# Kernel tuning notes

Hardware: AMD Instinct MI355X
Metric: run time of the kernel (lower is better)

The kernel has to match this reference:

```python
import jax, jax.numpy as jnp
import numpy as np

DIM = 512
QK_DIM = 128
HIDDEN = 2 * DIM  # expansion_factor * dim
EPS = 1e-5


def layernorm(x, scale, bias):
    mu = jnp.mean(x, axis=-1, keepdims=True)
    var = jnp.mean((x - mu) ** 2, axis=-1, keepdims=True)
    return (x - mu) * jax.lax.rsqrt(var + EPS) * scale + bias


def setup_inputs() -> dict:
    key = jax.random.key(0)
    ks = jax.random.split(key, 8)
    b, s = 4, 4096
    x = jax.random.normal(ks[0], (b, s, DIM), dtype=jnp.float32)
    inv = lambda fan_in: 1.0 / np.sqrt(fan_in)
    W_hidden = jax.random.normal(ks[1], (DIM, 2 * HIDDEN), dtype=jnp.float32) * inv(DIM)
    b_hidden = jnp.zeros((2 * HIDDEN,), dtype=jnp.float32)
    W_qk = jax.random.normal(ks[2], (DIM, QK_DIM), dtype=jnp.float32) * inv(DIM)
    b_qk = jnp.zeros((QK_DIM,), dtype=jnp.float32)
    gamma = jax.random.normal(ks[3], (2, QK_DIM), dtype=jnp.float32) * 0.02
    beta = jnp.zeros((2, QK_DIM), dtype=jnp.float32)
    W_out = jax.random.normal(ks[4], (HIDDEN, DIM), dtype=jnp.float32) * inv(HIDDEN)
    b_out = jnp.zeros((DIM,), dtype=jnp.float32)
    norm_scale = jnp.ones((DIM,), dtype=jnp.float32)
    norm_bias = jnp.zeros((DIM,), dtype=jnp.float32)
    return {
        "x": x,
        "norm_scale": norm_scale,
        "norm_bias": norm_bias,
        "W_hidden": W_hidden,
        "b_hidden": b_hidden,
        "W_qk": W_qk,
        "b_qk": b_qk,
        "gamma": gamma,
        "beta": beta,
        "W_out": W_out,
        "b_out": b_out,
    }


def reference(x, norm_scale, norm_bias, W_hidden, b_hidden, W_qk, b_qk, gamma, beta, W_out, b_out):
    seq_len = x.shape[-2]
    normed = layernorm(x, norm_scale, norm_bias)
    hidden = jax.nn.silu(normed @ W_hidden + b_hidden)          # [b, s, 2*hidden]
    v, gate = jnp.split(hidden, 2, axis=-1)                      # each [b, s, hidden]
    Z = jax.nn.silu(normed @ W_qk + b_qk)                        # [b, s, qk]
    QK = Z[..., None, :] * gamma + beta                          # [b, s, 2, qk]
    q = QK[..., 0, :]
    k = QK[..., 1, :]
    sim = jnp.einsum('bid,bjd->bij', q, k) / seq_len             # [b, s, s]
    A = jnp.square(jax.nn.relu(sim))
    V = jnp.einsum('bij,bjd->bid', A, v) * gate                  # [b, s, hidden]
    out = V @ W_out + b_out
    return out + x
```

## Files before the change

### kernel.cpp

```cpp
#include <hip/hip_runtime.h>
#include <cstdint>
#include <cstddef>

#define DIM   512
#define QKD   128
#define HID   1024
#define SEQ   4096
#define BAT   4
#define TOK   (BAT*SEQ)

typedef float f32x4 __attribute__((ext_vector_type(4)));
typedef int   i32x4 __attribute__((ext_vector_type(4)));
typedef int   i32x8 __attribute__((ext_vector_type(8)));

__device__ __forceinline__ unsigned short f2b(float f) {
    unsigned u = __builtin_bit_cast(unsigned, f);
    u += 0x7FFFu + ((u >> 16) & 1u);
    return (unsigned short)(u >> 16);
}
__device__ __forceinline__ float b2f(unsigned short h) {
    return __builtin_bit_cast(float, ((unsigned)h) << 16);
}
__device__ __forceinline__ float silu_f(float x) { return x / (1.f + __expf(-x)); }

__device__ __forceinline__ unsigned char f2e4(float f) {
    int v = __builtin_amdgcn_cvt_pk_fp8_f32(f, 0.f, 0, false);
    return (unsigned char)(v & 0xff);
}
__device__ __forceinline__ unsigned f2e4x4(float a, float b, float c, float d) {
    int w = __builtin_amdgcn_cvt_pk_fp8_f32(a, b, 0, false);
    w = __builtin_amdgcn_cvt_pk_fp8_f32(c, d, w, true);
    return (unsigned)w;
}

__device__ __forceinline__ void load16_lds(const void* gp, void* lp) {
    __builtin_amdgcn_global_load_lds(
        (const __attribute__((address_space(1))) unsigned int*)gp,
        (__attribute__((address_space(3))) unsigned int*)lp,
        16, 0, 0);
}

__global__ __launch_bounds__(256) void ln_kernel(
    const float* __restrict__ x, const float* __restrict__ sc,
    const float* __restrict__ bi, unsigned char* __restrict__ out)
{
    const int lane = threadIdx.x & 63, wid = threadIdx.x >> 6;
    const int row  = blockIdx.x * 4 + wid;
    const float4* xr = (const float4*)(x + (size_t)row * DIM);
    float4 a = xr[lane], b = xr[64 + lane];
    float s = a.x + a.y + a.z + a.w + b.x + b.y + b.z + b.w;
    float q = a.x*a.x + a.y*a.y + a.z*a.z + a.w*a.w
            + b.x*b.x + b.y*b.y + b.z*b.z + b.w*b.w;
#pragma unroll
    for (int m = 1; m < 64; m <<= 1) { s += __shfl_xor(s, m); q += __shfl_xor(q, m); }
    const float mean = s * (1.f / DIM);
    const float var  = q * (1.f / DIM) - mean * mean;
    const float rs   = rsqrtf(var + 1e-5f);
    float4 s0 = ((const float4*)sc)[lane], s1 = ((const float4*)sc)[64 + lane];
    float4 b0 = ((const float4*)bi)[lane], b1 = ((const float4*)bi)[64 + lane];
    unsigned wlo = f2e4x4((a.x - mean) * rs * s0.x + b0.x,
                          (a.y - mean) * rs * s0.y + b0.y,
                          (a.z - mean) * rs * s0.z + b0.z,
                          (a.w - mean) * rs * s0.w + b0.w);
    unsigned whi = f2e4x4((b.x - mean) * rs * s1.x + b1.x,
                          (b.y - mean) * rs * s1.y + b1.y,
                          (b.z - mean) * rs * s1.z + b1.z,
                          (b.w - mean) * rs * s1.w + b1.w);
    unsigned char* orow = out + (size_t)row * DIM;
    *(unsigned*)(orow + 4 * lane)       = wlo;
    *(unsigned*)(orow + 256 + 4 * lane) = whi;
}

__global__ __launch_bounds__(256) void tcast_f2e4_kernel(
    const float* __restrict__ in, unsigned char* __restrict__ out, int R, int C)
{
    __shared__ float t[32][33];
    const int tx = threadIdx.x & 31, ty = threadIdx.x >> 5;
    const int c0 = blockIdx.x * 32, r0 = blockIdx.y * 32;
#pragma unroll
    for (int i = 0; i < 4; ++i)
        t[ty + i * 8][tx] = in[(size_t)(r0 + ty + i * 8) * C + c0 + tx];
    __syncthreads();
#pragma unroll
    for (int i = 0; i < 4; ++i)
        out[(size_t)(c0 + ty + i * 8) * R + r0 + tx] = f2e4(t[tx][ty + i * 8] * 16.f);
}

__global__ __launch_bounds__(256) void copy_kernel(
    const float* __restrict__ in, float* __restrict__ out, int n4)
{
    int i = blockIdx.x * 256 + threadIdx.x;
    int stride = gridDim.x * 256;
    for (; i < n4; i += stride)
        ((float4*)out)[i] = ((const float4*)in)[i];
}

template<int EPI>
__global__ __launch_bounds__(256) void gemm8(
    const unsigned char* __restrict__ A, const unsigned char* __restrict__ B,
    int K, long strAz, long strBz, long strOz,
    const float* __restrict__ f0, const float* __restrict__ f1,
    const float* __restrict__ f2, const float* __restrict__ f3,
    const float* __restrict__ f4, const float* __restrict__ f5,
    unsigned short* __restrict__ gate,
    unsigned char* __restrict__ o0, unsigned char* __restrict__ o1,
    unsigned char* __restrict__ o2,
    float* __restrict__ fo, float scale)
{
    __shared__ unsigned char lds[32768];
    const int tid  = threadIdx.x;
    const int m0   = blockIdx.y * 128, n0 = blockIdx.x * 128;
    const int z    = blockIdx.z;
    A += (size_t)z * strAz;  B += (size_t)z * strBz;
    const int lane = tid & 63, wid = tid >> 6;
    const int wm   = (wid & 1) * 64, wn = (wid >> 1) * 64;
    const int l15  = lane & 15, quad = lane >> 4;

    f32x4 acc[4][4] = {};

    const int srow = tid >> 3, sseg = tid & 7;
    const unsigned char* gA = A + (size_t)(m0 + srow) * K + sseg * 16;
    const unsigned char* gB = B + (size_t)(n0 + srow) * K + sseg * 16;
    unsigned char* lA = lds + (size_t)tid * 16;
    unsigned char* lB = lds + 16384 + (size_t)tid * 16;

    for (int kt = 0; kt < K; kt += 128) {
#pragma unroll
        for (int i = 0; i < 4; ++i)
            load16_lds(gA + (size_t)i * 32 * K + kt, lA + i * 4096);
#pragma unroll
        for (int i = 0; i < 4; ++i)
            load16_lds(gB + (size_t)i * 32 * K + kt, lB + i * 4096);
        __syncthreads();
        i32x4 alo[4], ahi[4], blo[4], bhi[4];
#pragma unroll
        for (int mi = 0; mi < 4; ++mi) {
            const unsigned char* p = lds + (wm + mi * 16 + l15) * 128 + quad * 32;
            alo[mi] = *(const i32x4*)p; ahi[mi] = *(const i32x4*)(p + 16);
        }
#pragma unroll
        for (int ni = 0; ni < 4; ++ni) {
            const unsigned char* p = lds + 16384 + (wn + ni * 16 + l15) * 128 + quad * 32;
            blo[ni] = *(const i32x4*)p; bhi[ni] = *(const i32x4*)(p + 16);
        }
#pragma unroll
        for (int mi = 0; mi < 4; ++mi) {
            i32x8 af = __builtin_shufflevector(alo[mi], ahi[mi], 0,1,2,3,4,5,6,7);
#pragma unroll
            for (int ni = 0; ni < 4; ++ni) {
                i32x8 bf = __builtin_shufflevector(blo[ni], bhi[ni], 0,1,2,3,4,5,6,7);
                acc[mi][ni] = __builtin_amdgcn_mfma_scale_f32_16x16x128_f8f6f4(
                    af, bf, acc[mi][ni], 0, 0,
                    0, 0x7F7F7F7F, 0, 0x7F7F7F7F);
            }
        }
        __syncthreads();
    }

#pragma unroll
    for (int mi = 0; mi < 4; ++mi)
#pragma unroll
    for (int ni = 0; ni < 4; ++ni) {
        const int grow0 = m0 + wm + mi * 16 + quad * 4;
        const int gcol  = n0 + wn + ni * 16 + l15;
        if constexpr (EPI == 0) {
            if (gcol < HID) {
                const int b = grow0 >> 12, rloc = grow0 & (SEQ - 1);
                unsigned w = f2e4x4(silu_f(acc[mi][ni][0] * 0.0625f + f0[gcol]),
                                    silu_f(acc[mi][ni][1] * 0.0625f + f0[gcol]),
                                    silu_f(acc[mi][ni][2] * 0.0625f + f0[gcol]),
                                    silu_f(acc[mi][ni][3] * 0.0625f + f0[gcol]));
                *(unsigned*)(o0 + (size_t)b * HID * SEQ + (size_t)gcol * SEQ + rloc) = w;
            } else if (gcol < 2048) {
#pragma unroll
                for (int r = 0; r < 4; ++r)
                    gate[(size_t)(grow0 + r) * HID + (gcol - HID)] =
                        f2b(silu_f(acc[mi][ni][r] * 0.0625f + f0[gcol]));
            } else {
                const int c = gcol - 2048;
#pragma unroll
                for (int r = 0; r < 4; ++r) {
                    float zf = silu_f(acc[mi][ni][r] * 0.0625f + f1[c]);
                    o1[(size_t)(grow0 + r) * QKD + c] = f2e4((zf * f2[c] + f4[c]) * 64.f);
                    o2[(size_t)(grow0 + r) * QKD + c] = f2e4((zf * f3[c] + f5[c]) * 64.f);
                }
            }
        } else if constexpr (EPI == 1) {
            unsigned char* Ao = o0 + (size_t)z * strOz;
#pragma unroll
            for (int r = 0; r < 4; ++r) {
                float t = fmaxf(acc[mi][ni][r], 0.f) * 0.0625f;
                Ao[(size_t)(grow0 + r) * SEQ + gcol] = f2e4(t * t);
            }
        } else if constexpr (EPI == 2) {
            unsigned short* gz = gate + (size_t)z * strOz;
            unsigned char*  vo = o0 + (size_t)z * strOz;
#pragma unroll
            for (int r = 0; r < 4; ++r) {
                float g = b2f(gz[(size_t)(grow0 + r) * HID + gcol]);
                vo[(size_t)(grow0 + r) * HID + gcol] = f2e4(acc[mi][ni][r] * scale * g);
            }
        } else {
#pragma unroll
            for (int r = 0; r < 4; ++r)
                fo[(size_t)(grow0 + r) * DIM + gcol] =
                    acc[mi][ni][r] * scale + f0[gcol] + f1[(size_t)(grow0 + r) * DIM + gcol];
        }
    }
}

extern "C" void kernel_launch(void* const* d_in, const int* in_sizes, int n_in,
                              void* d_out, int out_size, void* d_ws, size_t ws_size,
                              hipStream_t stream) {
    const float* x     = (const float*)d_in[0];
    const float* nsc   = (const float*)d_in[1];
    const float* nbi   = (const float*)d_in[2];
    const float* Wh    = (const float*)d_in[3];
    const float* bh    = (const float*)d_in[4];
    const float* Wqk   = (const float*)d_in[5];
    const float* bqk   = (const float*)d_in[6];
    const float* gamma = (const float*)d_in[7];
    const float* beta  = (const float*)d_in[8];
    const float* Wout  = (const float*)d_in[9];
    const float* bout  = (const float*)d_in[10];
    float* out = (float*)d_out;

    uint8_t* ws = (uint8_t*)d_ws;
    size_t off = 0;
    auto alloc = [&](size_t n) { uint8_t* p = ws + off; off += (n + 255) & ~(size_t)255; return p; };
    unsigned char*  normed8 = (unsigned char*) alloc((size_t)TOK * DIM);
    unsigned char*  Wc8     = (unsigned char*) alloc((size_t)2176 * DIM);
    unsigned char*  Wout8   = (unsigned char*) alloc((size_t)DIM * HID);
    unsigned char*  vT8     = (unsigned char*) alloc((size_t)BAT * HID * SEQ);
    unsigned short* gbuf    = (unsigned short*)alloc((size_t)TOK * HID * 2);
    unsigned char*  q8      = (unsigned char*) alloc((size_t)TOK * QKD);
    unsigned char*  k8      = (unsigned char*) alloc((size_t)TOK * QKD);
    unsigned char*  Ab8     = (unsigned char*) alloc((size_t)BAT * SEQ * SEQ);
    unsigned char*  vg8     = (unsigned char*) alloc((size_t)TOK * HID);

    if (ws_size < off) {
        copy_kernel<<<4096, 256, 0, stream>>>(x, out, TOK * DIM / 4);
        return;
    }

    ln_kernel<<<TOK / 4, 256, 0, stream>>>(x, nsc, nbi, normed8);
    tcast_f2e4_kernel<<<dim3(2048 / 32, DIM / 32), 256, 0, stream>>>(Wh, Wc8, DIM, 2048);
    tcast_f2e4_kernel<<<dim3(QKD / 32, DIM / 32), 256, 0, stream>>>(
        Wqk, Wc8 + (size_t)2048 * DIM, DIM, QKD);
    tcast_f2e4_kernel<<<dim3(DIM / 32, HID / 32), 256, 0, stream>>>(Wout, Wout8, HID, DIM);

    gemm8<0><<<dim3(2176 / 128, TOK / 128), 256, 0, stream>>>(
        normed8, Wc8, DIM, 0, 0, 0,
        bh, bqk, gamma, gamma + QKD, beta, beta + QKD,
        gbuf, vT8, q8, k8, nullptr, 0.f);

    gemm8<1><<<dim3(SEQ / 128, SEQ / 128, BAT), 256, 0, stream>>>(
        q8, k8, QKD, (long)SEQ * QKD, (long)SEQ * QKD, (long)SEQ * SEQ,
        nullptr, nullptr, nullptr, nullptr, nullptr, nullptr,
        nullptr, Ab8, nullptr, nullptr, nullptr, 0.f);

    gemm8<2><<<dim3(HID / 128, SEQ / 128, BAT), 256, 0, stream>>>(
        Ab8, vT8, SEQ, (long)SEQ * SEQ, (long)HID * SEQ, (long)SEQ * HID,
        nullptr, nullptr, nullptr, nullptr, nullptr, nullptr,
        gbuf, vg8, nullptr, nullptr, nullptr, 0x1p-12f);

    gemm8<3><<<dim3(DIM / 128, TOK / 128), 256, 0, stream>>>(
        vg8, Wout8, HID, 0, 0, 0,
        bout, x, nullptr, nullptr, nullptr, nullptr,
        nullptr, nullptr, nullptr, nullptr, out, 0x1p-32f);
}
```

Before: 314.3 us.

## Template GEMM on K-tile depth, swizzle block order, store gate as fp8

```diff
diff --git a/kernel.cpp b/kernel.cpp
--- a/kernel.cpp
+++ b/kernel.cpp
@@ -18,9 +18,6 @@
     u += 0x7FFFu + ((u >> 16) & 1u);
     return (unsigned short)(u >> 16);
 }
-__device__ __forceinline__ float b2f(unsigned short h) {
-    return __builtin_bit_cast(float, ((unsigned)h) << 16);
-}
 __device__ __forceinline__ float silu_f(float x) { return x / (1.f + __expf(-x)); }
 
 __device__ __forceinline__ unsigned char f2e4(float f) {
@@ -31,6 +28,9 @@
     int w = __builtin_amdgcn_cvt_pk_fp8_f32(a, b, 0, false);
     w = __builtin_amdgcn_cvt_pk_fp8_f32(c, d, w, true);
     return (unsigned)w;
+}
+__device__ __forceinline__ float e42f(unsigned char b) {
+    return __builtin_amdgcn_cvt_f32_fp8((int)b, 0);
 }
 
 __device__ __forceinline__ void load16_lds(const void* gp, void* lp) {
@@ -95,22 +95,29 @@
         ((float4*)out)[i] = ((const float4*)in)[i];
 }
 
-template<int EPI>
+template<int EPI, int BK, int NX>
 __global__ __launch_bounds__(256) void gemm8(
     const unsigned char* __restrict__ A, const unsigned char* __restrict__ B,
     int K, long strAz, long strBz, long strOz,
     const float* __restrict__ f0, const float* __restrict__ f1,
     const float* __restrict__ f2, const float* __restrict__ f3,
     const float* __restrict__ f4, const float* __restrict__ f5,
-    unsigned short* __restrict__ gate,
+    unsigned char* __restrict__ gate,
     unsigned char* __restrict__ o0, unsigned char* __restrict__ o1,
     unsigned char* __restrict__ o2,
     float* __restrict__ fo, float scale)
 {
-    __shared__ unsigned char lds[32768];
-    const int tid  = threadIdx.x;
-    const int m0   = blockIdx.y * 128, n0 = blockIdx.x * 128;
-    const int z    = blockIdx.z;
+    constexpr int TPR = BK / 16;
+    constexpr int RPI = 256 / TPR;
+    constexpr int NIS = 128 / RPI;
+    __shared__ unsigned char lds[2 * 128 * BK];
+
+    const int tid = threadIdx.x;
+    const int d  = blockIdx.x + NX * blockIdx.y;
+    const int qd = d >> 3;
+    const int m0 = ((d & 7) + 8 * (qd / NX)) * 128;
+    const int n0 = (qd % NX) * 128;
+    const int z  = blockIdx.z;
     A += (size_t)z * strAz;  B += (size_t)z * strBz;
     const int lane = tid & 63, wid = tid >> 6;
     const int wm   = (wid & 1) * 64, wn = (wid >> 1) * 64;
@@ -118,40 +125,43 @@
 
     f32x4 acc[4][4] = {};
 
-    const int srow = tid >> 3, sseg = tid & 7;
+    const int srow = tid / TPR, sseg = tid % TPR;
     const unsigned char* gA = A + (size_t)(m0 + srow) * K + sseg * 16;
     const unsigned char* gB = B + (size_t)(n0 + srow) * K + sseg * 16;
     unsigned char* lA = lds + (size_t)tid * 16;
-    unsigned char* lB = lds + 16384 + (size_t)tid * 16;
-
-    for (int kt = 0; kt < K; kt += 128) {
-#pragma unroll
-        for (int i = 0; i < 4; ++i)
-            load16_lds(gA + (size_t)i * 32 * K + kt, lA + i * 4096);
-#pragma unroll
-        for (int i = 0; i < 4; ++i)
-            load16_lds(gB + (size_t)i * 32 * K + kt, lB + i * 4096);
+    unsigned char* lB = lds + 128 * BK + (size_t)tid * 16;
+
+    for (int kt = 0; kt < K; kt += BK) {
+#pragma unroll
+        for (int i = 0; i < NIS; ++i)
+            load16_lds(gA + (size_t)i * RPI * K + kt, lA + i * 4096);
+#pragma unroll
+        for (int i = 0; i < NIS; ++i)
+            load16_lds(gB + (size_t)i * RPI * K + kt, lB + i * 4096);
         __syncthreads();
-        i32x4 alo[4], ahi[4], blo[4], bhi[4];
-#pragma unroll
-        for (int mi = 0; mi < 4; ++mi) {
-            const unsigned char* p = lds + (wm + mi * 16 + l15) * 128 + quad * 32;
-            alo[mi] = *(const i32x4*)p; ahi[mi] = *(const i32x4*)(p + 16);
-        }
-#pragma unroll
-        for (int ni = 0; ni < 4; ++ni) {
-            const unsigned char* p = lds + 16384 + (wn + ni * 16 + l15) * 128 + quad * 32;
-            blo[ni] = *(const i32x4*)p; bhi[ni] = *(const i32x4*)(p + 16);
-        }
-#pragma unroll
-        for (int mi = 0; mi < 4; ++mi) {
-            i32x8 af = __builtin_shufflevector(alo[mi], ahi[mi], 0,1,2,3,4,5,6,7);
+#pragma unroll
+        for (int kk = 0; kk < BK; kk += 128) {
+            i32x4 alo[4], ahi[4], blo[4], bhi[4];
+#pragma unroll
+            for (int mi = 0; mi < 4; ++mi) {
+                const unsigned char* p = lds + (size_t)(wm + mi * 16 + l15) * BK + kk + quad * 32;
+                alo[mi] = *(const i32x4*)p; ahi[mi] = *(const i32x4*)(p + 16);
+            }
 #pragma unroll
             for (int ni = 0; ni < 4; ++ni) {
-                i32x8 bf = __builtin_shufflevector(blo[ni], bhi[ni], 0,1,2,3,4,5,6,7);
-                acc[mi][ni] = __builtin_amdgcn_mfma_scale_f32_16x16x128_f8f6f4(
-                    af, bf, acc[mi][ni], 0, 0,
-                    0, 0x7F7F7F7F, 0, 0x7F7F7F7F);
+                const unsigned char* p = lds + 128 * BK + (size_t)(wn + ni * 16 + l15) * BK + kk + quad * 32;
+                blo[ni] = *(const i32x4*)p; bhi[ni] = *(const i32x4*)(p + 16);
+            }
+#pragma unroll
+            for (int mi = 0; mi < 4; ++mi) {
+                i32x8 af = __builtin_shufflevector(alo[mi], ahi[mi], 0,1,2,3,4,5,6,7);
+#pragma unroll
+                for (int ni = 0; ni < 4; ++ni) {
+                    i32x8 bf = __builtin_shufflevector(blo[ni], bhi[ni], 0,1,2,3,4,5,6,7);
+                    acc[mi][ni] = __builtin_amdgcn_mfma_scale_f32_16x16x128_f8f6f4(
+                        af, bf, acc[mi][ni], 0, 0,
+                        0, 0x7F7F7F7F, 0, 0x7F7F7F7F);
+                }
             }
         }
         __syncthreads();
@@ -175,7 +185,7 @@
 #pragma unroll
                 for (int r = 0; r < 4; ++r)
                     gate[(size_t)(grow0 + r) * HID + (gcol - HID)] =
-                        f2b(silu_f(acc[mi][ni][r] * 0.0625f + f0[gcol]));
+                        f2e4(silu_f(acc[mi][ni][r] * 0.0625f + f0[gcol]));
             } else {
                 const int c = gcol - 2048;
 #pragma unroll
@@ -193,11 +203,11 @@
                 Ao[(size_t)(grow0 + r) * SEQ + gcol] = f2e4(t * t);
             }
         } else if constexpr (EPI == 2) {
-            unsigned short* gz = gate + (size_t)z * strOz;
-            unsigned char*  vo = o0 + (size_t)z * strOz;
+            unsigned char* gz = gate + (size_t)z * strOz;
+            unsigned char* vo = o0 + (size_t)z * strOz;
 #pragma unroll
             for (int r = 0; r < 4; ++r) {
-                float g = b2f(gz[(size_t)(grow0 + r) * HID + gcol]);
+                float g = e42f(gz[(size_t)(grow0 + r) * HID + gcol]);
                 vo[(size_t)(grow0 + r) * HID + gcol] = f2e4(acc[mi][ni][r] * scale * g);
             }
         } else {
@@ -228,15 +238,15 @@
     uint8_t* ws = (uint8_t*)d_ws;
     size_t off = 0;
     auto alloc = [&](size_t n) { uint8_t* p = ws + off; off += (n + 255) & ~(size_t)255; return p; };
-    unsigned char*  normed8 = (unsigned char*) alloc((size_t)TOK * DIM);
-    unsigned char*  Wc8     = (unsigned char*) alloc((size_t)2176 * DIM);
-    unsigned char*  Wout8   = (unsigned char*) alloc((size_t)DIM * HID);
-    unsigned char*  vT8     = (unsigned char*) alloc((size_t)BAT * HID * SEQ);
-    unsigned short* gbuf    = (unsigned short*)alloc((size_t)TOK * HID * 2);
-    unsigned char*  q8      = (unsigned char*) alloc((size_t)TOK * QKD);
-    unsigned char*  k8      = (unsigned char*) alloc((size_t)TOK * QKD);
-    unsigned char*  Ab8     = (unsigned char*) alloc((size_t)BAT * SEQ * SEQ);
-    unsigned char*  vg8     = (unsigned char*) alloc((size_t)TOK * HID);
+    unsigned char* normed8 = (unsigned char*)alloc((size_t)TOK * DIM);
+    unsigned char* Wc8     = (unsigned char*)alloc((size_t)2176 * DIM);
+    unsigned char* Wout8   = (unsigned char*)alloc((size_t)DIM * HID);
+    unsigned char* vT8     = (unsigned char*)alloc((size_t)BAT * HID * SEQ);
+    unsigned char* gbuf    = (unsigned char*)alloc((size_t)TOK * HID);
+    unsigned char* q8      = (unsigned char*)alloc((size_t)TOK * QKD);
+    unsigned char* k8      = (unsigned char*)alloc((size_t)TOK * QKD);
+    unsigned char* Ab8     = (unsigned char*)alloc((size_t)BAT * SEQ * SEQ);
+    unsigned char* vg8     = (unsigned char*)alloc((size_t)TOK * HID);
 
     if (ws_size < off) {
         copy_kernel<<<4096, 256, 0, stream>>>(x, out, TOK * DIM / 4);
@@ -249,22 +259,22 @@
         Wqk, Wc8 + (size_t)2048 * DIM, DIM, QKD);
     tcast_f2e4_kernel<<<dim3(DIM / 32, HID / 32), 256, 0, stream>>>(Wout, Wout8, HID, DIM);
 
-    gemm8<0><<<dim3(2176 / 128, TOK / 128), 256, 0, stream>>>(
+    gemm8<0, 256, 17><<<dim3(17, TOK / 128), 256, 0, stream>>>(
         normed8, Wc8, DIM, 0, 0, 0,
         bh, bqk, gamma, gamma + QKD, beta, beta + QKD,
         gbuf, vT8, q8, k8, nullptr, 0.f);
 
-    gemm8<1><<<dim3(SEQ / 128, SEQ / 128, BAT), 256, 0, stream>>>(
+    gemm8<1, 128, 32><<<dim3(SEQ / 128, SEQ / 128, BAT), 256, 0, stream>>>(
         q8, k8, QKD, (long)SEQ * QKD, (long)SEQ * QKD, (long)SEQ * SEQ,
         nullptr, nullptr, nullptr, nullptr, nullptr, nullptr,
         nullptr, Ab8, nullptr, nullptr, nullptr, 0.f);
 
-    gemm8<2><<<dim3(HID / 128, SEQ / 128, BAT), 256, 0, stream>>>(
+    gemm8<2, 256, 8><<<dim3(HID / 128, SEQ / 128, BAT), 256, 0, stream>>>(
         Ab8, vT8, SEQ, (long)SEQ * SEQ, (long)HID * SEQ, (long)SEQ * HID,
         nullptr, nullptr, nullptr, nullptr, nullptr, nullptr,
         gbuf, vg8, nullptr, nullptr, nullptr, 0x1p-12f);
 
-    gemm8<3><<<dim3(DIM / 128, TOK / 128), 256, 0, stream>>>(
+    gemm8<3, 256, 4><<<dim3(DIM / 128, TOK / 128), 256, 0, stream>>>(
         vg8, Wout8, HID, 0, 0, 0,
         bout, x, nullptr, nullptr, nullptr, nullptr,
         nullptr, nullptr, nullptr, nullptr, out, 0x1p-32f);
```

After: 363.5 us. +15.6%, slower.
